# Performance work log

Measured on AMD Instinct MI355X. Metric: run time of the kernel, lower is better.

Reference implementation:

```python
import jax, jax.numpy as jnp
import numpy as np

# BlendParams defaults (pytorch3d) and camera clip planes from the module
SIGMA = 1e-4
GAMMA = 1e-4
BACKGROUND = (1.0, 1.0, 1.0)
ZNEAR = 1.0
ZFAR = 100.0
EPS = 1e-10

N, H, W, K = 4, 512, 512, 8
F, V = 100000, 50000


def setup_inputs() -> dict:
    key = jax.random.key(0)
    k1, k2, k3, k4, k5, k6 = jax.random.split(key, 6)
    bary = jax.random.uniform(k1, (N, H, W, K, 3), dtype=jnp.float32)
    bary = bary / jnp.sum(bary, axis=-1, keepdims=True)  # valid barycentric coords
    # depth buffer values inside [znear, zfar]
    zbuf = ZNEAR + (ZFAR - ZNEAR) * jax.random.uniform(k2, (N, H, W, K), dtype=jnp.float32)
    # signed squared distances to face edges, small magnitude (rasterizer blur region)
    dists = 1e-4 * jax.random.normal(k3, (N, H, W, K), dtype=jnp.float32)
    vn = jax.random.normal(k4, (V, 3), dtype=jnp.float32)
    verts_normals = vn / jnp.linalg.norm(vn, axis=-1, keepdims=True)
    # -1 marks background pixels (no face rasterized into that slot)
    pix_to_face = jax.random.randint(k5, (N, H, W, K), -1, F, dtype=jnp.int32)
    faces = jax.random.randint(k6, (F, 3), 0, V, dtype=jnp.int32)
    return {
        "bary_coords": bary,
        "zbuf": zbuf,
        "dists": dists,
        "verts_normals": verts_normals,
        "pix_to_face": pix_to_face,
        "faces": faces,
    }


def _shade_and_blend(bary_coords, zbuf, dists, verts_normals, pix_to_face, faces):
    mask = pix_to_face >= 0                       # [N,H,W,K]
    p2f = jnp.where(mask, pix_to_face, 0)
    # world_normal_shading: interpolate_face_attributes(pix_to_face, bary, verts_normals[faces])
    face_vert_normals = verts_normals[faces]      # [F,3,3] (3 verts, 3 components)
    pix_attrs = face_vert_normals[p2f]            # [N,H,W,K,3,3]
    colors = jnp.einsum("nhwkv,nhwkvc->nhwkc", bary_coords, pix_attrs)
    colors = jnp.where(mask[..., None], colors, 0.0)  # zero out empty fragments

    # softmax_rgb_blend (pytorch3d)
    maskf = mask.astype(colors.dtype)
    prob_map = jax.nn.sigmoid(-dists / SIGMA) * maskf          # [N,H,W,K]
    alpha = 1.0 - jnp.prod(1.0 - prob_map, axis=-1)            # [N,H,W]
    z_inv = (ZFAR - zbuf) / (ZFAR - ZNEAR) * maskf             # [N,H,W,K]
    z_inv_max = jnp.maximum(jnp.max(z_inv, axis=-1, keepdims=True), EPS)
    weights_num = prob_map * jnp.exp((z_inv - z_inv_max) / GAMMA)
    delta = jnp.exp((EPS - z_inv_max) / GAMMA)                 # [N,H,W,1]
    denom = jnp.sum(weights_num, axis=-1, keepdims=True) + delta
    weighted_colors = jnp.einsum("nhwk,nhwkc->nhwc", weights_num, colors) / denom
    background = jnp.asarray(BACKGROUND, dtype=colors.dtype)
    weighted_background = (delta / denom) * background         # [N,H,W,3]
    rgb = weighted_colors + weighted_background
    return jnp.concatenate([rgb, alpha[..., None]], axis=-1)   # [N,H,W,4]


def reference(bary_coords, zbuf, dists, verts_normals, pix_to_face, faces):
    return _shade_and_blend(bary_coords, zbuf, dists, verts_normals, pix_to_face, faces)
```

## Files before the change

kernel.cpp:

```cpp
#include <hip/hip_runtime.h>
#include <hip/hip_fp16.h>

#define K 8

static __device__ __forceinline__ unsigned pack2(float lo, float hi) {
    __half2 h = __floats2half2_rn(lo, hi);
    return *reinterpret_cast<unsigned*>(&h);
}
static __device__ __forceinline__ float2 unpack2(unsigned u) {
    __half2 h = *reinterpret_cast<__half2*>(&u);
    return __half22float2(h);
}

__global__ __launch_bounds__(256) void pack_face_normals(
    const int*   __restrict__ faces,
    const float* __restrict__ vn,
    uint4*       __restrict__ tbl,
    int F)
{
    int f = blockIdx.x * blockDim.x + threadIdx.x;
    if (f >= F) return;
    int v0 = faces[3 * f + 0];
    int v1 = faces[3 * f + 1];
    int v2 = faces[3 * f + 2];
    float n0x = vn[3 * v0 + 0], n0y = vn[3 * v0 + 1], n0z = vn[3 * v0 + 2];
    float n1x = vn[3 * v1 + 0], n1y = vn[3 * v1 + 1], n1z = vn[3 * v1 + 2];
    float n2x = vn[3 * v2 + 0], n2y = vn[3 * v2 + 1], n2z = vn[3 * v2 + 2];
    uint4 a, b;
    a.x = pack2(n0x, n0y);
    a.y = pack2(n0z, n1x);
    a.z = pack2(n1y, n1z);
    a.w = pack2(n2x, n2y);
    b.x = pack2(n2z, 0.0f);
    b.y = 0u; b.z = 0u; b.w = 0u;
    tbl[2 * f + 0] = a;
    tbl[2 * f + 1] = b;
}

__global__ __launch_bounds__(256) void shade_blend_packed(
    const float*    __restrict__ bary,
    const float*    __restrict__ zbuf,
    const float*    __restrict__ dists,
    const int*      __restrict__ p2f,
    const uint4*    __restrict__ tbl,
    float*          __restrict__ out,
    int P)
{
    const float SIGMA_INV = 1e4f;
    const float GAMMA_INV = 1e4f;
    const float EPSV      = 1e-10f;
    const float ZFAR      = 100.0f;
    const float ZSCALE    = 1.0f / 99.0f;

    int pix = blockIdx.x * blockDim.x + threadIdx.x;
    if (pix >= P) return;

    const float4* zb4 = reinterpret_cast<const float4*>(zbuf  + (size_t)pix * K);
    const float4* ds4 = reinterpret_cast<const float4*>(dists + (size_t)pix * K);
    const int4*   pf4 = reinterpret_cast<const int4*>(p2f     + (size_t)pix * K);
    const float4* bc4 = reinterpret_cast<const float4*>(bary  + (size_t)pix * K * 3);
    const unsigned* tbl32 = reinterpret_cast<const unsigned*>(tbl);

    float4 za = zb4[0], zb_ = zb4[1];
    float4 da = ds4[0], db_ = ds4[1];
    int4   fa = pf4[0], fb_ = pf4[1];

    float zk[K] = { za.x, za.y, za.z, za.w, zb_.x, zb_.y, zb_.z, zb_.w };
    float dk[K] = { da.x, da.y, da.z, da.w, db_.x, db_.y, db_.z, db_.w };
    int   fk[K] = { fa.x, fa.y, fa.z, fa.w, fb_.x, fb_.y, fb_.z, fb_.w };

    float barr[K * 3];
#pragma unroll
    for (int i = 0; i < 6; ++i) {
        float4 t = bc4[i];
        barr[4 * i + 0] = t.x;
        barr[4 * i + 1] = t.y;
        barr[4 * i + 2] = t.z;
        barr[4 * i + 3] = t.w;
    }

    float prob[K], zinv[K], c0[K], c1[K], c2[K];
    float zmax = EPSV;

#pragma unroll
    for (int k = 0; k < K; ++k) {
        int fraw = fk[k];
        float mf = fraw >= 0 ? 1.0f : 0.0f;
        int fi = fraw >= 0 ? fraw : 0;

        uint4    ra = tbl[2 * fi];
        unsigned rb = tbl32[8 * fi + 4];

        float p = 1.0f / (1.0f + __expf(dk[k] * SIGMA_INV));
        prob[k] = p * mf;
        zinv[k] = (ZFAR - zk[k]) * ZSCALE * mf;
        zmax = fmaxf(zmax, zinv[k]);

        float2 p01 = unpack2(ra.x);
        float2 p23 = unpack2(ra.y);
        float2 p45 = unpack2(ra.z);
        float2 p67 = unpack2(ra.w);
        float2 p8  = unpack2(rb);
        float b0 = barr[3 * k + 0] * mf;
        float b1 = barr[3 * k + 1] * mf;
        float b2 = barr[3 * k + 2] * mf;
        c0[k] = b0 * p01.x + b1 * p23.y + b2 * p67.x;
        c1[k] = b0 * p01.y + b1 * p45.x + b2 * p67.y;
        c2[k] = b0 * p23.x + b1 * p45.y + b2 * p8.x;
    }

    float one_minus_prod = 1.0f;
    float wsum = 0.0f, a0 = 0.0f, a1 = 0.0f, a2 = 0.0f;
#pragma unroll
    for (int k = 0; k < K; ++k) {
        one_minus_prod *= (1.0f - prob[k]);
        float w = prob[k] * __expf((zinv[k] - zmax) * GAMMA_INV);
        wsum += w;
        a0 += w * c0[k];
        a1 += w * c1[k];
        a2 += w * c2[k];
    }
    float delta = __expf((EPSV - zmax) * GAMMA_INV);
    float inv_denom = 1.0f / (wsum + delta);
    float bgw = delta * inv_denom;

    float4 o;
    o.x = a0 * inv_denom + bgw;
    o.y = a1 * inv_denom + bgw;
    o.z = a2 * inv_denom + bgw;
    o.w = 1.0f - one_minus_prod;
    *reinterpret_cast<float4*>(out + (size_t)pix * 4) = o;
}

__global__ __launch_bounds__(256) void shade_blend_direct(
    const float* __restrict__ bary, const float* __restrict__ zbuf,
    const float* __restrict__ dists, const float* __restrict__ vn,
    const int* __restrict__ p2f, const int* __restrict__ faces,
    float* __restrict__ out, int P)
{
    const float SIGMA_INV = 1e4f, GAMMA_INV = 1e4f, EPSV = 1e-10f;
    const float ZFAR = 100.0f, ZSCALE = 1.0f / 99.0f;
    int pix = blockIdx.x * blockDim.x + threadIdx.x;
    if (pix >= P) return;
    const float4* zb4 = reinterpret_cast<const float4*>(zbuf  + (size_t)pix * K);
    const float4* ds4 = reinterpret_cast<const float4*>(dists + (size_t)pix * K);
    const int4*   pf4 = reinterpret_cast<const int4*>(p2f     + (size_t)pix * K);
    const float4* bc4 = reinterpret_cast<const float4*>(bary  + (size_t)pix * K * 3);
    float4 za = zb4[0], zb_ = zb4[1];
    float4 da = ds4[0], db_ = ds4[1];
    int4   fa = pf4[0], fb_ = pf4[1];
    float zk[K] = { za.x, za.y, za.z, za.w, zb_.x, zb_.y, zb_.z, zb_.w };
    float dk[K] = { da.x, da.y, da.z, da.w, db_.x, db_.y, db_.z, db_.w };
    int   fk[K] = { fa.x, fa.y, fa.z, fa.w, fb_.x, fb_.y, fb_.z, fb_.w };
    float barr[K * 3];
#pragma unroll
    for (int i = 0; i < 6; ++i) {
        float4 t = bc4[i];
        barr[4 * i + 0] = t.x; barr[4 * i + 1] = t.y;
        barr[4 * i + 2] = t.z; barr[4 * i + 3] = t.w;
    }
    float prob[K], zinv[K], c0[K], c1[K], c2[K];
    float zmax = EPSV;
#pragma unroll
    for (int k = 0; k < K; ++k) {
        int fraw = fk[k];
        float mf = fraw >= 0 ? 1.0f : 0.0f;
        int fi = fraw >= 0 ? fraw : 0;
        int v0 = faces[3 * fi + 0], v1 = faces[3 * fi + 1], v2 = faces[3 * fi + 2];
        float p = 1.0f / (1.0f + __expf(dk[k] * SIGMA_INV));
        prob[k] = p * mf;
        zinv[k] = (ZFAR - zk[k]) * ZSCALE * mf;
        zmax = fmaxf(zmax, zinv[k]);
        float b0 = barr[3 * k + 0] * mf, b1 = barr[3 * k + 1] * mf, b2 = barr[3 * k + 2] * mf;
        c0[k] = b0 * vn[3 * v0 + 0] + b1 * vn[3 * v1 + 0] + b2 * vn[3 * v2 + 0];
        c1[k] = b0 * vn[3 * v0 + 1] + b1 * vn[3 * v1 + 1] + b2 * vn[3 * v2 + 1];
        c2[k] = b0 * vn[3 * v0 + 2] + b1 * vn[3 * v1 + 2] + b2 * vn[3 * v2 + 2];
    }
    float one_minus_prod = 1.0f, wsum = 0.0f, a0 = 0.0f, a1 = 0.0f, a2 = 0.0f;
#pragma unroll
    for (int k = 0; k < K; ++k) {
        one_minus_prod *= (1.0f - prob[k]);
        float w = prob[k] * __expf((zinv[k] - zmax) * GAMMA_INV);
        wsum += w; a0 += w * c0[k]; a1 += w * c1[k]; a2 += w * c2[k];
    }
    float delta = __expf((EPSV - zmax) * GAMMA_INV);
    float inv_denom = 1.0f / (wsum + delta);
    float bgw = delta * inv_denom;
    float4 o;
    o.x = a0 * inv_denom + bgw; o.y = a1 * inv_denom + bgw;
    o.z = a2 * inv_denom + bgw; o.w = 1.0f - one_minus_prod;
    *reinterpret_cast<float4*>(out + (size_t)pix * 4) = o;
}

extern "C" void kernel_launch(void* const* d_in, const int* in_sizes, int n_in,
                              void* d_out, int out_size, void* d_ws, size_t ws_size,
                              hipStream_t stream) {
    const float* bary  = (const float*)d_in[0];
    const float* zbuf  = (const float*)d_in[1];
    const float* dists = (const float*)d_in[2];
    const float* vn    = (const float*)d_in[3];
    const int*   p2f   = (const int*)d_in[4];
    const int*   faces = (const int*)d_in[5];
    float* out = (float*)d_out;

    int P = out_size / 4;
    int F = in_sizes[5] / 3;
    int block = 256;
    int grid = (P + block - 1) / block;

    size_t tbl_bytes = (size_t)F * 32;
    if (ws_size >= tbl_bytes) {
        uint4* tbl = (uint4*)d_ws;
        int gf = (F + block - 1) / block;
        pack_face_normals<<<gf, block, 0, stream>>>(faces, vn, tbl, F);
        shade_blend_packed<<<grid, block, 0, stream>>>(bary, zbuf, dists, p2f, tbl, out, P);
    } else {
        shade_blend_direct<<<grid, block, 0, stream>>>(bary, zbuf, dists, vn, p2f, faces, out, P);
    }
}
```

Before: 304.6 us.

## Quantize face normals to 10-bit packed records and use nontemporal streaming loads

```diff
diff --git a/kernel.cpp b/kernel.cpp
--- a/kernel.cpp
+++ b/kernel.cpp
@@ -1,21 +1,20 @@
 #include <hip/hip_runtime.h>
-#include <hip/hip_fp16.h>
 
 #define K 8
 
-static __device__ __forceinline__ unsigned pack2(float lo, float hi) {
-    __half2 h = __floats2half2_rn(lo, hi);
-    return *reinterpret_cast<unsigned*>(&h);
-}
-static __device__ __forceinline__ float2 unpack2(unsigned u) {
-    __half2 h = *reinterpret_cast<__half2*>(&u);
-    return __half22float2(h);
-}
-
-__global__ __launch_bounds__(256) void pack_face_normals(
+typedef float    f32x4 __attribute__((ext_vector_type(4)));
+typedef int      i32x4 __attribute__((ext_vector_type(4)));
+typedef unsigned u32x4 __attribute__((ext_vector_type(4)));
+
+static __device__ __forceinline__ unsigned quant10(float v) {
+    v = fminf(fmaxf(v, -1.0f), 1.0f);
+    return (unsigned)__float2uint_rn((v + 1.0f) * 511.5f);
+}
+
+__global__ __launch_bounds__(256) void pack_face_normals_q10(
     const int*   __restrict__ faces,
     const float* __restrict__ vn,
-    uint4*       __restrict__ tbl,
+    u32x4*       __restrict__ tbl,
     int F)
 {
     int f = blockIdx.x * blockDim.x + threadIdx.x;
@@ -23,27 +22,26 @@
     int v0 = faces[3 * f + 0];
     int v1 = faces[3 * f + 1];
     int v2 = faces[3 * f + 2];
-    float n0x = vn[3 * v0 + 0], n0y = vn[3 * v0 + 1], n0z = vn[3 * v0 + 2];
-    float n1x = vn[3 * v1 + 0], n1y = vn[3 * v1 + 1], n1z = vn[3 * v1 + 2];
-    float n2x = vn[3 * v2 + 0], n2y = vn[3 * v2 + 1], n2z = vn[3 * v2 + 2];
-    uint4 a, b;
-    a.x = pack2(n0x, n0y);
-    a.y = pack2(n0z, n1x);
-    a.z = pack2(n1y, n1z);
-    a.w = pack2(n2x, n2y);
-    b.x = pack2(n2z, 0.0f);
-    b.y = 0u; b.z = 0u; b.w = 0u;
-    tbl[2 * f + 0] = a;
-    tbl[2 * f + 1] = b;
-}
-
-__global__ __launch_bounds__(256) void shade_blend_packed(
-    const float*    __restrict__ bary,
-    const float*    __restrict__ zbuf,
-    const float*    __restrict__ dists,
-    const int*      __restrict__ p2f,
-    const uint4*    __restrict__ tbl,
-    float*          __restrict__ out,
+    u32x4 r;
+    r.x = quant10(vn[3 * v0 + 0]) | (quant10(vn[3 * v0 + 1]) << 10) | (quant10(vn[3 * v0 + 2]) << 20);
+    r.y = quant10(vn[3 * v1 + 0]) | (quant10(vn[3 * v1 + 1]) << 10) | (quant10(vn[3 * v1 + 2]) << 20);
+    r.z = quant10(vn[3 * v2 + 0]) | (quant10(vn[3 * v2 + 1]) << 10) | (quant10(vn[3 * v2 + 2]) << 20);
+    r.w = 0u;
+    tbl[f] = r;
+}
+
+static __device__ __forceinline__ float dq(unsigned w, int shift) {
+    const float S = 2.0f / 1023.0f;
+    return (float)((w >> shift) & 1023u) * S - 1.0f;
+}
+
+__global__ __launch_bounds__(256) void shade_blend_q10(
+    const float* __restrict__ bary,
+    const float* __restrict__ zbuf,
+    const float* __restrict__ dists,
+    const int*   __restrict__ p2f,
+    const u32x4* __restrict__ tbl,
+    float*       __restrict__ out,
     int P)
 {
     const float SIGMA_INV = 1e4f;
@@ -55,15 +53,17 @@
     int pix = blockIdx.x * blockDim.x + threadIdx.x;
     if (pix >= P) return;
 
-    const float4* zb4 = reinterpret_cast<const float4*>(zbuf  + (size_t)pix * K);
-    const float4* ds4 = reinterpret_cast<const float4*>(dists + (size_t)pix * K);
-    const int4*   pf4 = reinterpret_cast<const int4*>(p2f     + (size_t)pix * K);
-    const float4* bc4 = reinterpret_cast<const float4*>(bary  + (size_t)pix * K * 3);
-    const unsigned* tbl32 = reinterpret_cast<const unsigned*>(tbl);
-
-    float4 za = zb4[0], zb_ = zb4[1];
-    float4 da = ds4[0], db_ = ds4[1];
-    int4   fa = pf4[0], fb_ = pf4[1];
+    const f32x4* zb4 = reinterpret_cast<const f32x4*>(zbuf  + (size_t)pix * K);
+    const f32x4* ds4 = reinterpret_cast<const f32x4*>(dists + (size_t)pix * K);
+    const i32x4* pf4 = reinterpret_cast<const i32x4*>(p2f   + (size_t)pix * K);
+    const f32x4* bc4 = reinterpret_cast<const f32x4*>(bary  + (size_t)pix * K * 3);
+
+    f32x4 za  = __builtin_nontemporal_load(zb4 + 0);
+    f32x4 zb_ = __builtin_nontemporal_load(zb4 + 1);
+    f32x4 da  = __builtin_nontemporal_load(ds4 + 0);
+    f32x4 db_ = __builtin_nontemporal_load(ds4 + 1);
+    i32x4 fa  = __builtin_nontemporal_load(pf4 + 0);
+    i32x4 fb_ = __builtin_nontemporal_load(pf4 + 1);
 
     float zk[K] = { za.x, za.y, za.z, za.w, zb_.x, zb_.y, zb_.z, zb_.w };
     float dk[K] = { da.x, da.y, da.z, da.w, db_.x, db_.y, db_.z, db_.w };
@@ -72,41 +72,39 @@
     float barr[K * 3];
 #pragma unroll
     for (int i = 0; i < 6; ++i) {
-        float4 t = bc4[i];
+        f32x4 t = __builtin_nontemporal_load(bc4 + i);
         barr[4 * i + 0] = t.x;
         barr[4 * i + 1] = t.y;
         barr[4 * i + 2] = t.z;
         barr[4 * i + 3] = t.w;
     }
 
+    u32x4 rec[K];
+#pragma unroll
+    for (int k = 0; k < K; ++k) {
+        int fi = fk[k] >= 0 ? fk[k] : 0;
+        rec[k] = tbl[fi];
+    }
+
     float prob[K], zinv[K], c0[K], c1[K], c2[K];
     float zmax = EPSV;
 
 #pragma unroll
     for (int k = 0; k < K; ++k) {
-        int fraw = fk[k];
-        float mf = fraw >= 0 ? 1.0f : 0.0f;
-        int fi = fraw >= 0 ? fraw : 0;
-
-        uint4    ra = tbl[2 * fi];
-        unsigned rb = tbl32[8 * fi + 4];
+        float mf = fk[k] >= 0 ? 1.0f : 0.0f;
 
         float p = 1.0f / (1.0f + __expf(dk[k] * SIGMA_INV));
         prob[k] = p * mf;
         zinv[k] = (ZFAR - zk[k]) * ZSCALE * mf;
         zmax = fmaxf(zmax, zinv[k]);
 
-        float2 p01 = unpack2(ra.x);
-        float2 p23 = unpack2(ra.y);
-        float2 p45 = unpack2(ra.z);
-        float2 p67 = unpack2(ra.w);
-        float2 p8  = unpack2(rb);
+        unsigned w0 = rec[k].x, w1 = rec[k].y, w2 = rec[k].z;
         float b0 = barr[3 * k + 0] * mf;
         float b1 = barr[3 * k + 1] * mf;
         float b2 = barr[3 * k + 2] * mf;
-        c0[k] = b0 * p01.x + b1 * p23.y + b2 * p67.x;
-        c1[k] = b0 * p01.y + b1 * p45.x + b2 * p67.y;
-        c2[k] = b0 * p23.x + b1 * p45.y + b2 * p8.x;
+        c0[k] = b0 * dq(w0, 0)  + b1 * dq(w1, 0)  + b2 * dq(w2, 0);
+        c1[k] = b0 * dq(w0, 10) + b1 * dq(w1, 10) + b2 * dq(w2, 10);
+        c2[k] = b0 * dq(w0, 20) + b1 * dq(w1, 20) + b2 * dq(w2, 20);
     }
 
     float one_minus_prod = 1.0f;
@@ -124,12 +122,12 @@
     float inv_denom = 1.0f / (wsum + delta);
     float bgw = delta * inv_denom;
 
-    float4 o;
+    f32x4 o;
     o.x = a0 * inv_denom + bgw;
     o.y = a1 * inv_denom + bgw;
     o.z = a2 * inv_denom + bgw;
     o.w = 1.0f - one_minus_prod;
-    *reinterpret_cast<float4*>(out + (size_t)pix * 4) = o;
+    __builtin_nontemporal_store(o, reinterpret_cast<f32x4*>(out + (size_t)pix * 4));
 }
 
 __global__ __launch_bounds__(256) void shade_blend_direct(
@@ -208,12 +206,12 @@
     int block = 256;
     int grid = (P + block - 1) / block;
 
-    size_t tbl_bytes = (size_t)F * 32;
+    size_t tbl_bytes = (size_t)F * 16;
     if (ws_size >= tbl_bytes) {
-        uint4* tbl = (uint4*)d_ws;
+        u32x4* tbl = (u32x4*)d_ws;
         int gf = (F + block - 1) / block;
-        pack_face_normals<<<gf, block, 0, stream>>>(faces, vn, tbl, F);
-        shade_blend_packed<<<grid, block, 0, stream>>>(bary, zbuf, dists, p2f, tbl, out, P);
+        pack_face_normals_q10<<<gf, block, 0, stream>>>(faces, vn, tbl, F);
+        shade_blend_q10<<<grid, block, 0, stream>>>(bary, zbuf, dists, p2f, tbl, out, P);
     } else {
         shade_blend_direct<<<grid, block, 0, stream>>>(bary, zbuf, dists, vn, p2f, faces, out, P);
     }
```

Result: faster. 279.1 us (-8.4%).
